# Kernel optimization log

Hardware: AMD Instinct MI355X
Metric: run time of the kernel (lower is better)

## Reference

```python
import jax, jax.numpy as jnp
import numpy as np

D = 1024
H = 16
F = 4096
EPS = 1e-6


def _layernorm(x, alpha, bias):
    # Faithful to torch: unbiased std (ddof=1), divide by (std + eps)
    mean = jnp.mean(x, axis=-1, keepdims=True)
    std = jnp.std(x, axis=-1, keepdims=True, ddof=1)
    return alpha * (x - mean) / (std + EPS) + bias


def setup_inputs() -> dict:
    key = jax.random.key(0)
    ks = jax.random.split(key, 12)
    B, S = 2, 2048
    s = 1.0 / np.sqrt(D)
    inp = {
        "x": jax.random.normal(ks[0], (B, S, D), jnp.float32),
        "mask": jnp.ones((B, 1, 1, S), jnp.int32),
        "wq": jax.random.normal(ks[1], (D, D), jnp.float32) * s,
        "bq": jnp.zeros((D,), jnp.float32),
        "wk": jax.random.normal(ks[2], (D, D), jnp.float32) * s,
        "bk": jnp.zeros((D,), jnp.float32),
        "wv": jax.random.normal(ks[3], (D, D), jnp.float32) * s,
        "bv": jnp.zeros((D,), jnp.float32),
        "wo": jax.random.normal(ks[4], (D, D), jnp.float32) * s,
        "bo": jnp.zeros((D,), jnp.float32),
        "ln1_a": jnp.ones((D,), jnp.float32),
        "ln1_b": jnp.zeros((D,), jnp.float32),
        "ln2_a": jnp.ones((D,), jnp.float32),
        "ln2_b": jnp.zeros((D,), jnp.float32),
        "w1": jax.random.normal(ks[5], (D, F), jnp.float32) * s,
        "b1": jnp.zeros((F,), jnp.float32),
        "w2": jax.random.normal(ks[6], (F, D), jnp.float32) * (1.0 / np.sqrt(F)),
        "b2": jnp.zeros((D,), jnp.float32),
    }
    return inp


def reference(x, mask, wq, bq, wk, bk, wv, bv, wo, bo,
              ln1_a, ln1_b, ln2_a, ln2_b, w1, b1, w2, b2):
    B, S, _ = x.shape
    dk = D // H
    # --- residual 1: pre-LN self-attention ---
    h = _layernorm(x, ln1_a, ln1_b)
    q = (h @ wq + bq).reshape(B, S, H, dk).transpose(0, 2, 1, 3)
    k = (h @ wk + bk).reshape(B, S, H, dk).transpose(0, 2, 1, 3)
    v = (h @ wv + bv).reshape(B, S, H, dk).transpose(0, 2, 1, 3)
    scores = jnp.einsum('bhqd,bhkd->bhqk', q, k) / jnp.sqrt(jnp.float32(dk))
    scores = jnp.where(mask == 0, jnp.float32(-1e9), scores)
    attn = jax.nn.softmax(scores, axis=-1)
    ctx = jnp.einsum('bhqk,bhkd->bhqd', attn, v)
    ctx = ctx.transpose(0, 2, 1, 3).reshape(B, S, D)
    x = x + (ctx @ wo + bo)
    # --- residual 2: pre-LN feed-forward ---
    h = _layernorm(x, ln2_a, ln2_b)
    ff = jax.nn.relu(h @ w1 + b1) @ w2 + b2
    return x + ff
```

## Files before the change

kernel.cpp:

```cpp
#include <hip/hip_runtime.h>
#include <hip/hip_bf16.h>
#include <math.h>

typedef __attribute__((ext_vector_type(8))) short bf16x8;
typedef __attribute__((ext_vector_type(4))) float f32x4;
typedef unsigned int uint32;
typedef __attribute__((ext_vector_type(2))) unsigned int uint32x2;

#define DMODEL 1024
#define SEQ    2048
#define NB     2
#define NH     16
#define HD     64
#define FDIM   4096
#define NTOK   (NB*SEQ)

__device__ __forceinline__ void async16(const void* g, void* s) {
    __builtin_amdgcn_global_load_lds((const __attribute__((address_space(1))) unsigned int*)g,
                                     (__attribute__((address_space(3))) unsigned int*)s,
                                     16, 0, 0);
}

__global__ __launch_bounds__(256) void transpose_cvt_k(const float* __restrict__ src,
                                                       __hip_bfloat16* __restrict__ dst,
                                                       int R, int C) {
    __shared__ __hip_bfloat16 tile[32][33];
    int tx = threadIdx.x, ty = threadIdx.y;
    int bx = blockIdx.x * 32, by = blockIdx.y * 32;
    for (int i = 0; i < 32; i += 8)
        tile[ty + i][tx] = __float2bfloat16(src[(size_t)(by + ty + i) * C + bx + tx]);
    __syncthreads();
    for (int i = 0; i < 32; i += 8)
        dst[(size_t)(bx + ty + i) * R + by + tx] = tile[tx][ty + i];
}

__global__ __launch_bounds__(256) void transpose_cvt4_k(const float* __restrict__ s0,
                                                        const float* __restrict__ s1,
                                                        const float* __restrict__ s2,
                                                        const float* __restrict__ s3,
                                                        __hip_bfloat16* __restrict__ d012,
                                                        __hip_bfloat16* __restrict__ d3) {
    __shared__ __hip_bfloat16 tile[32][33];
    const int z = blockIdx.z;
    const float* src = (z == 0) ? s0 : (z == 1) ? s1 : (z == 2) ? s2 : s3;
    __hip_bfloat16* dst = (z < 3) ? d012 + (size_t)z * DMODEL * DMODEL : d3;
    int tx = threadIdx.x, ty = threadIdx.y;
    int bx = blockIdx.x * 32, by = blockIdx.y * 32;
    for (int i = 0; i < 32; i += 8)
        tile[ty + i][tx] = __float2bfloat16(src[(size_t)(by + ty + i) * DMODEL + bx + tx]);
    __syncthreads();
    for (int i = 0; i < 32; i += 8)
        dst[(size_t)(bx + ty + i) * DMODEL + by + tx] = tile[tx][ty + i];
}

__global__ __launch_bounds__(256) void ln_kernel(const float* __restrict__ x,
                                                 const float* __restrict__ alpha,
                                                 const float* __restrict__ beta,
                                                 __hip_bfloat16* __restrict__ out) {
    const int row = blockIdx.x, tid = threadIdx.x;
    const size_t base = (size_t)row * DMODEL;
    float v[4];
    for (int e = 0; e < 4; ++e) v[e] = x[base + tid * 4 + e];
    float s1 = v[0] + v[1] + v[2] + v[3];
    float s2 = v[0]*v[0] + v[1]*v[1] + v[2]*v[2] + v[3]*v[3];
    for (int off = 32; off > 0; off >>= 1) {
        s1 += __shfl_down(s1, off);
        s2 += __shfl_down(s2, off);
    }
    __shared__ float red[8];
    int w = tid >> 6, lane = tid & 63;
    if (lane == 0) { red[w * 2] = s1; red[w * 2 + 1] = s2; }
    __syncthreads();
    if (tid == 0) {
        float a = 0.f, b = 0.f;
        for (int i = 0; i < 4; ++i) { a += red[2 * i]; b += red[2 * i + 1]; }
        red[0] = a; red[1] = b;
    }
    __syncthreads();
    s1 = red[0]; s2 = red[1];
    float mean = s1 * (1.0f / DMODEL);
    float var  = fmaxf((s2 - (float)DMODEL * mean * mean) * (1.0f / (DMODEL - 1)), 0.f);
    float inv  = 1.0f / (sqrtf(var) + 1e-6f);
    for (int e = 0; e < 4; ++e) {
        int c = tid * 4 + e;
        float y = alpha[c] * (v[e] - mean) * inv + beta[c];
        out[base + c] = __float2bfloat16(y);
    }
}

template <int EPI>
__global__ __launch_bounds__(256) void gemm_bt(const __hip_bfloat16* __restrict__ A,
                                               const __hip_bfloat16* __restrict__ Bt,
                                               const float* __restrict__ bias,
                                               const float* __restrict__ res,
                                               void* __restrict__ Cout,
                                               int M, int N, int K) {
    __shared__ alignas(16) __hip_bfloat16 As[2][128 * 32];
    __shared__ alignas(16) __hip_bfloat16 Bs[2][128 * 32];
    const int tid = threadIdx.x, l = tid & 63;
    const int w = tid >> 6;
    const int wm = w >> 1, wn = w & 1, quad = l >> 4, lc = l & 15;
    const int row0 = blockIdx.y * 128, col0 = blockIdx.x * 128;
    const int lr = l >> 2, cb = l & 3;
    const int srow = 32 * w + lr;
    const int scol = (cb ^ ((lr >> 1) & 3)) * 8;
    const int rsw  = (lc >> 1) & 3;

    f32x4 acc[4][4];
    for (int i = 0; i < 4; ++i)
        for (int j = 0; j < 4; ++j) acc[i][j] = (f32x4){0.f, 0.f, 0.f, 0.f};

    for (int c = 0; c < 2; ++c) {
        async16(A  + (size_t)(row0 + srow + 16 * c) * K + scol, (char*)&As[0][0] + w * 2048 + c * 1024);
        async16(Bt + (size_t)(col0 + srow + 16 * c) * K + scol, (char*)&Bs[0][0] + w * 2048 + c * 1024);
    }
    const int NKT = K / 32;
    for (int kt = 0; kt < NKT; ++kt) {
        const int cur = kt & 1;
        __syncthreads();
        if (kt + 1 < NKT) {
            const int k1 = (kt + 1) * 32;
            for (int c = 0; c < 2; ++c) {
                async16(A  + (size_t)(row0 + srow + 16 * c) * K + k1 + scol, (char*)&As[cur ^ 1][0] + w * 2048 + c * 1024);
                async16(Bt + (size_t)(col0 + srow + 16 * c) * K + k1 + scol, (char*)&Bs[cur ^ 1][0] + w * 2048 + c * 1024);
            }
        }
        bf16x8 af[4], bfr[4];
        for (int i = 0; i < 4; ++i) af[i]  = *(const bf16x8*)&As[cur][(64 * wm + 16 * i + lc) * 32 + (quad ^ rsw) * 8];
        for (int j = 0; j < 4; ++j) bfr[j] = *(const bf16x8*)&Bs[cur][(64 * wn + 16 * j + lc) * 32 + (quad ^ rsw) * 8];
        for (int i = 0; i < 4; ++i)
            for (int j = 0; j < 4; ++j)
                acc[i][j] = __builtin_amdgcn_mfma_f32_16x16x32_bf16(af[i], bfr[j], acc[i][j], 0, 0, 0);
    }

    __hip_bfloat16* Cb = (__hip_bfloat16*)Cout;
    float* Cf = (float*)Cout;
    for (int j = 0; j < 4; ++j) {
        int col = col0 + 64 * wn + 16 * j + lc;
        float bv = bias[col];
        for (int i = 0; i < 4; ++i) {
            int rbase = row0 + 64 * wm + 16 * i + quad * 4;
            for (int r = 0; r < 4; ++r) {
                size_t idx = (size_t)(rbase + r) * N + col;
                float vacc = acc[i][j][r] + bv;
                if (EPI == 0)      Cb[idx] = __float2bfloat16(vacc);
                else if (EPI == 1) Cb[idx] = __float2bfloat16(fmaxf(vacc, 0.f));
                else               Cf[idx] = vacc + res[idx];
            }
        }
    }
}

template <int EPI>
__global__ __launch_bounds__(512) void gemm_bt_sk(const __hip_bfloat16* __restrict__ A,
                                                  const __hip_bfloat16* __restrict__ Bt,
                                                  const float* __restrict__ bias,
                                                  const float* __restrict__ res,
                                                  void* __restrict__ Cout,
                                                  int M, int N, int K) {
    __shared__ alignas(16) char smem[65536];
    const int tid = threadIdx.x, l = tid & 63;
    const int w = tid >> 6;
    const int g = w >> 2;
    const int wl = w & 3;
    const int wm = wl >> 1, wn = wl & 1, quad = l >> 4, lc = l & 15;
    const int row0 = blockIdx.y * 128, col0 = blockIdx.x * 128;
    const int lr = l >> 2, cb = l & 3;
    const int srow = 32 * wl + lr;
    const int scol = (cb ^ ((lr >> 1) & 3)) * 8;
    const int rsw  = (lc >> 1) & 3;
    const int Kh = K >> 1;
    const int kbase = g * Kh;

    char* AsBase = smem + (size_t)g * 16384;
    char* BsBase = smem + 32768 + (size_t)g * 16384;

    f32x4 acc[4][4];
    for (int i = 0; i < 4; ++i)
        for (int j = 0; j < 4; ++j) acc[i][j] = (f32x4){0.f, 0.f, 0.f, 0.f};

    for (int c = 0; c < 2; ++c) {
        async16(A  + (size_t)(row0 + srow + 16 * c) * K + kbase + scol, AsBase + wl * 2048 + c * 1024);
        async16(Bt + (size_t)(col0 + srow + 16 * c) * K + kbase + scol, BsBase + wl * 2048 + c * 1024);
    }
    const int NKT = Kh / 32;
    for (int kt = 0; kt < NKT; ++kt) {
        const int cur = kt & 1;
        __syncthreads();
        if (kt + 1 < NKT) {
            const int k1 = kbase + (kt + 1) * 32;
            for (int c = 0; c < 2; ++c) {
                async16(A  + (size_t)(row0 + srow + 16 * c) * K + k1 + scol, AsBase + (cur ^ 1) * 8192 + wl * 2048 + c * 1024);
                async16(Bt + (size_t)(col0 + srow + 16 * c) * K + k1 + scol, BsBase + (cur ^ 1) * 8192 + wl * 2048 + c * 1024);
            }
        }
        const __hip_bfloat16* Asc = (const __hip_bfloat16*)(AsBase + cur * 8192);
        const __hip_bfloat16* Bsc = (const __hip_bfloat16*)(BsBase + cur * 8192);
        bf16x8 af[4], bfr[4];
        for (int i = 0; i < 4; ++i) af[i]  = *(const bf16x8*)&Asc[(64 * wm + 16 * i + lc) * 32 + (quad ^ rsw) * 8];
        for (int j = 0; j < 4; ++j) bfr[j] = *(const bf16x8*)&Bsc[(64 * wn + 16 * j + lc) * 32 + (quad ^ rsw) * 8];
        for (int i = 0; i < 4; ++i)
            for (int j = 0; j < 4; ++j)
                acc[i][j] = __builtin_amdgcn_mfma_f32_16x16x32_bf16(af[i], bfr[j], acc[i][j], 0, 0, 0);
    }

    __syncthreads();
    float* comb = (float*)smem;
    if (g == 1) {
        for (int j = 0; j < 4; ++j) {
            int col = 64 * wn + 16 * j + lc;
            int ccol = col ^ ((quad & 1) << 4);
            for (int i = 0; i < 4; ++i) {
                int rb = 64 * wm + 16 * i + quad * 4;
                for (int r = 0; r < 4; ++r)
                    comb[(rb + r) * 128 + ccol] = acc[i][j][r];
            }
        }
    }
    __syncthreads();
    if (g == 0) {
        __hip_bfloat16* Cb = (__hip_bfloat16*)Cout;
        float* Cf = (float*)Cout;
        for (int j = 0; j < 4; ++j) {
            int coll = 64 * wn + 16 * j + lc;
            int ccol = coll ^ ((quad & 1) << 4);
            int col  = col0 + coll;
            float bv = bias[col];
            for (int i = 0; i < 4; ++i) {
                int rbl = 64 * wm + 16 * i + quad * 4;
                for (int r = 0; r < 4; ++r) {
                    size_t idx = (size_t)(row0 + rbl + r) * N + col;
                    float vacc = acc[i][j][r] + comb[(rbl + r) * 128 + ccol] + bv;
                    if (EPI == 0)      Cb[idx] = __float2bfloat16(vacc);
                    else if (EPI == 1) Cb[idx] = __float2bfloat16(fmaxf(vacc, 0.f));
                    else               Cf[idx] = vacc + res[idx];
                }
            }
        }
    }
}

__global__ __launch_bounds__(256) void gemm_qkv(const __hip_bfloat16* __restrict__ A,
                                                const __hip_bfloat16* __restrict__ Bt,
                                                const float* __restrict__ bq,
                                                const float* __restrict__ bk,
                                                const float* __restrict__ bv,
                                                __hip_bfloat16* __restrict__ qout,
                                                __hip_bfloat16* __restrict__ kout,
                                                __hip_bfloat16* __restrict__ vTout) {
    const int K = DMODEL;
    __shared__ alignas(16) __hip_bfloat16 As[2][128 * 32];
    __shared__ alignas(16) __hip_bfloat16 Bs[2][128 * 32];
    const int tid = threadIdx.x, l = tid & 63;
    const int w = tid >> 6;
    const int wm = w >> 1, wn = w & 1, quad = l >> 4, lc = l & 15;
    const int row0 = blockIdx.y * 128, col0 = blockIdx.x * 128;
    const int lr = l >> 2, cb = l & 3;
    const int srow = 32 * w + lr;
    const int scol = (cb ^ ((lr >> 1) & 3)) * 8;
    const int rsw  = (lc >> 1) & 3;

    f32x4 acc[4][4];
    for (int i = 0; i < 4; ++i)
        for (int j = 0; j < 4; ++j) acc[i][j] = (f32x4){0.f, 0.f, 0.f, 0.f};

    for (int c = 0; c < 2; ++c) {
        async16(A  + (size_t)(row0 + srow + 16 * c) * K + scol, (char*)&As[0][0] + w * 2048 + c * 1024);
        async16(Bt + (size_t)(col0 + srow + 16 * c) * K + scol, (char*)&Bs[0][0] + w * 2048 + c * 1024);
    }
    const int NKT = K / 32;
    for (int kt = 0; kt < NKT; ++kt) {
        const int cur = kt & 1;
        __syncthreads();
        if (kt + 1 < NKT) {
            const int k1 = (kt + 1) * 32;
            for (int c = 0; c < 2; ++c) {
                async16(A  + (size_t)(row0 + srow + 16 * c) * K + k1 + scol, (char*)&As[cur ^ 1][0] + w * 2048 + c * 1024);
                async16(Bt + (size_t)(col0 + srow + 16 * c) * K + k1 + scol, (char*)&Bs[cur ^ 1][0] + w * 2048 + c * 1024);
            }
        }
        bf16x8 af[4], bfr[4];
        for (int i = 0; i < 4; ++i) af[i]  = *(const bf16x8*)&As[cur][(64 * wm + 16 * i + lc) * 32 + (quad ^ rsw) * 8];
        for (int j = 0; j < 4; ++j) bfr[j] = *(const bf16x8*)&Bs[cur][(64 * wn + 16 * j + lc) * 32 + (quad ^ rsw) * 8];
        for (int i = 0; i < 4; ++i)
            for (int j = 0; j < 4; ++j)
                acc[i][j] = __builtin_amdgcn_mfma_f32_16x16x32_bf16(af[i], bfr[j], acc[i][j], 0, 0, 0);
    }

    const int seg = col0 >> 10;
    const float* bias = (seg == 0) ? bq : (seg == 1) ? bk : bv;
    for (int j = 0; j < 4; ++j) {
        int col  = col0 + 64 * wn + 16 * j + lc;
        int colm = col & (DMODEL - 1);
        float bvx = bias[colm];
        for (int i = 0; i < 4; ++i) {
            int rbase = row0 + 64 * wm + 16 * i + quad * 4;
            for (int r = 0; r < 4; ++r) {
                int trow = rbase + r;
                float vacc = acc[i][j][r] + bvx;
                if (seg == 2) {
                    int bb = trow >> 11, s = trow & (SEQ - 1);
                    int hh = colm >> 6, d = colm & (HD - 1);
                    vTout[((size_t)(bb * NH + hh) * HD + d) * SEQ + s] = __float2bfloat16(vacc);
                } else {
                    __hip_bfloat16* dst = (seg == 0) ? qout : kout;
                    dst[(size_t)trow * DMODEL + colm] = __float2bfloat16(vacc);
                }
            }
        }
    }
}

__global__ __launch_bounds__(512) void attn_kernel(const __hip_bfloat16* __restrict__ q,
                                                   const __hip_bfloat16* __restrict__ k,
                                                   const __hip_bfloat16* __restrict__ vT,
                                                   const int* __restrict__ mask,
                                                   __hip_bfloat16* __restrict__ ctx) {
    const int qt = blockIdx.x, bh = blockIdx.y;
    const int b = bh >> 4;
    const int q0 = qt * 128;
    const int tid = threadIdx.x, w = tid >> 6, l = tid & 63, quad = l >> 4, lc = l & 15;
    const int g = w >> 2, wl = w & 3;

    __shared__ alignas(16) char smem[65536];
    __hip_bfloat16* KhB = (__hip_bfloat16*)(smem + (size_t)g * 32768);
    __hip_bfloat16* VhB = (__hip_bfloat16*)(smem + (size_t)g * 32768 + 16384);

    const size_t base   = (size_t)b * SEQ * DMODEL + (size_t)(bh & 15) * HD;
    const size_t vtbase = (size_t)bh * HD * SEQ;
    const int gk = g * (SEQ / 2);

    bf16x8 qf[2][2];
    for (int s = 0; s < 2; ++s) {
        const __hip_bfloat16* qrow = &q[base + (size_t)(q0 + s * 64 + wl * 16 + lc) * DMODEL];
        qf[s][0] = *(const bf16x8*)&qrow[quad * 8];
        qf[s][1] = *(const bf16x8*)&qrow[32 + quad * 8];
    }

    f32x4 o[2][4];
    for (int s = 0; s < 2; ++s)
        for (int dj = 0; dj < 4; ++dj) o[s][dj] = (f32x4){0.f, 0.f, 0.f, 0.f};
    float rsp2[2] = {0.f, 0.f};

    const int lr  = l >> 2, cb = l & 3;
    const int cbsw = ((cb ^ ((lr >> 1) & 3))) * 8;
    const int rsw  = (lc >> 1) & 3;

    for (int c = 0; c < 2; ++c) {
        const int W = wl * 2 + c;
        const int rr = (W & 3) * 16 + lr, cc8 = (W >> 2) * 32 + cbsw;
        async16(&k [base   + (size_t)(gk + rr) * DMODEL + cc8], (char*)KhB + W * 1024);
        async16(&vT[vtbase + (size_t)rr * SEQ + gk + cc8],      (char*)VhB + W * 1024);
    }

    const int NT = SEQ / 128;
    for (int kt = 0; kt < NT; ++kt) {
        const int k0 = gk + kt * 64;
        const int cur = kt & 1;

        __syncthreads();
        if (kt + 1 < NT) {
            const int k1 = k0 + 64;
            for (int c = 0; c < 2; ++c) {
                const int W = wl * 2 + c;
                const int rr = (W & 3) * 16 + lr, cc8 = (W >> 2) * 32 + cbsw;
                async16(&k [base   + (size_t)(k1 + rr) * DMODEL + cc8], (char*)KhB + (cur ^ 1) * 8192 + W * 1024);
                async16(&vT[vtbase + (size_t)rr * SEQ + k1 + cc8],      (char*)VhB + (cur ^ 1) * 8192 + W * 1024);
            }
        }
        float mb[4][4];
        for (int jn = 0; jn < 4; ++jn) {
            int4 mi = *(const int4*)&mask[b * SEQ + k0 + jn * 16 + quad * 4];
            mb[jn][0] = mi.x ? 0.f : -INFINITY;
            mb[jn][1] = mi.y ? 0.f : -INFINITY;
            mb[jn][2] = mi.z ? 0.f : -INFINITY;
            mb[jn][3] = mi.w ? 0.f : -INFINITY;
        }

        bf16x8 kf0[4], kf1[4];
        for (int jn = 0; jn < 4; ++jn) {
            kf0[jn] = *(const bf16x8*)&KhB[(cur * 2 + 0) * 2048 + (jn * 16 + lc) * 32 + (quad ^ rsw) * 8];
            kf1[jn] = *(const bf16x8*)&KhB[(cur * 2 + 1) * 2048 + (jn * 16 + lc) * 32 + (quad ^ rsw) * 8];
        }
        bf16x8 vf0[4], vf1[4];
        for (int dj = 0; dj < 4; ++dj) {
            vf0[dj] = *(const bf16x8*)&VhB[(cur * 2 + 0) * 2048 + (dj * 16 + lc) * 32 + (quad ^ rsw) * 8];
            vf1[dj] = *(const bf16x8*)&VhB[(cur * 2 + 1) * 2048 + (dj * 16 + lc) * 32 + (quad ^ rsw) * 8];
        }

        for (int s = 0; s < 2; ++s) {
            f32x4 sa[4];
            __builtin_amdgcn_s_setprio(1);
            for (int jn = 0; jn < 4; ++jn) {
                f32x4 z = (f32x4){0.f, 0.f, 0.f, 0.f};
                z = __builtin_amdgcn_mfma_f32_16x16x32_bf16(kf0[jn], qf[s][0], z, 0, 0, 0);
                z = __builtin_amdgcn_mfma_f32_16x16x32_bf16(kf1[jn], qf[s][1], z, 0, 0, 0);
                sa[jn] = z;
            }
            __builtin_amdgcn_s_setprio(0);

            uint32 wd[4][2];
            float accs = 0.f;
            for (int jn = 0; jn < 4; ++jn) {
                float p0 = __expf(fmaf(sa[jn][0], 0.125f, mb[jn][0]));
                float p1 = __expf(fmaf(sa[jn][1], 0.125f, mb[jn][1]));
                float p2 = __expf(fmaf(sa[jn][2], 0.125f, mb[jn][2]));
                float p3 = __expf(fmaf(sa[jn][3], 0.125f, mb[jn][3]));
                accs += (p0 + p1) + (p2 + p3);
                __hip_bfloat16 h0 = __float2bfloat16(p0), h1 = __float2bfloat16(p1);
                __hip_bfloat16 h2 = __float2bfloat16(p2), h3 = __float2bfloat16(p3);
                wd[jn][0] = (uint32)*(unsigned short*)&h0 | ((uint32)*(unsigned short*)&h1 << 16);
                wd[jn][1] = (uint32)*(unsigned short*)&h2 | ((uint32)*(unsigned short*)&h3 << 16);
            }
            rsp2[s] += accs;

            union { uint32 u[4]; bf16x8 v8; } pf0, pf1;
            for (int p = 0; p < 2; ++p) {
                uint32x2 a = __builtin_amdgcn_permlane32_swap(wd[0][p], wd[1][p], false, false);
                uint32x2 r = __builtin_amdgcn_permlane16_swap(a[0], a[1], false, false);
                pf0.u[p] = r[0]; pf0.u[2 + p] = r[1];
                uint32x2 a2 = __builtin_amdgcn_permlane32_swap(wd[2][p], wd[3][p], false, false);
                uint32x2 r2 = __builtin_amdgcn_permlane16_swap(a2[0], a2[1], false, false);
                pf1.u[p] = r2[0]; pf1.u[2 + p] = r2[1];
            }

            __builtin_amdgcn_s_setprio(1);
            for (int dj = 0; dj < 4; ++dj) {
                o[s][dj] = __builtin_amdgcn_mfma_f32_16x16x32_bf16(pf0.v8, vf0[dj], o[s][dj], 0, 0, 0);
                o[s][dj] = __builtin_amdgcn_mfma_f32_16x16x32_bf16(pf1.v8, vf1[dj], o[s][dj], 0, 0, 0);
            }
            __builtin_amdgcn_s_setprio(0);
        }
    }

    __syncthreads();
    float* combo = (float*)smem;
    float* crs   = (float*)(smem + 33792);
    if (g == 1) {
        for (int s = 0; s < 2; ++s) {
            crs[(wl * 64 + l) * 2 + s] = rsp2[s];
            for (int dj = 0; dj < 4; ++dj)
                for (int r = 0; r < 4; ++r)
                    combo[(s * 64 + wl * 16 + quad * 4 + r) * 66 + dj * 16 + lc] = o[s][dj][r];
        }
    }
    __syncthreads();
    if (g == 0) {
        for (int s = 0; s < 2; ++s) {
            float rs = rsp2[s] + crs[(wl * 64 + l) * 2 + s];
            rs += __shfl_xor(rs, 16);
            rs += __shfl_xor(rs, 32);
            for (int r = 0; r < 4; ++r) {
                float rq = __shfl(rs, (l & 48) | (quad * 4 + r));
                float linv = 1.0f / rq;
                int row = q0 + s * 64 + wl * 16 + quad * 4 + r;
                for (int dj = 0; dj < 4; ++dj) {
                    float ov = o[s][dj][r] + combo[(s * 64 + wl * 16 + quad * 4 + r) * 66 + dj * 16 + lc];
                    ctx[base + (size_t)row * DMODEL + dj * 16 + lc] = __float2bfloat16(ov * linv);
                }
            }
        }
    }
}

extern "C" void kernel_launch(void* const* d_in, const int* in_sizes, int n_in,
                              void* d_out, int out_size, void* d_ws, size_t ws_size,
                              hipStream_t stream) {
    const float* x    = (const float*)d_in[0];
    const int*   mask = (const int*)d_in[1];
    const float* wq = (const float*)d_in[2];
    const float* bq = (const float*)d_in[3];
    const float* wk = (const float*)d_in[4];
    const float* bk = (const float*)d_in[5];
    const float* wv = (const float*)d_in[6];
    const float* bv = (const float*)d_in[7];
    const float* wo = (const float*)d_in[8];
    const float* bo = (const float*)d_in[9];
    const float* ln1_a = (const float*)d_in[10];
    const float* ln1_b = (const float*)d_in[11];
    const float* ln2_a = (const float*)d_in[12];
    const float* ln2_b = (const float*)d_in[13];
    const float* w1 = (const float*)d_in[14];
    const float* b1 = (const float*)d_in[15];
    const float* w2 = (const float*)d_in[16];
    const float* b2 = (const float*)d_in[17];
    float* out = (float*)d_out;

    char* ws = (char*)d_ws;
    const size_t SZ_WT  = (size_t)DMODEL * DMODEL * 2;
    const size_t SZ_ACT = (size_t)NTOK * DMODEL * 2;
    const size_t SZ_WF  = (size_t)FDIM * DMODEL * 2;
    size_t off = 0;
    __hip_bfloat16* wqkvT = (__hip_bfloat16*)(ws + off); off += 3 * SZ_WT;
    __hip_bfloat16* woT   = (__hip_bfloat16*)(ws + off); off += SZ_WT;
    __hip_bfloat16* w1T   = (__hip_bfloat16*)(ws + off); off += SZ_WF;
    __hip_bfloat16* w2T   = (__hip_bfloat16*)(ws + off); off += SZ_WF;
    __hip_bfloat16* h1    = (__hip_bfloat16*)(ws + off); off += SZ_ACT;
    __hip_bfloat16* qb    = (__hip_bfloat16*)(ws + off); off += SZ_ACT;
    __hip_bfloat16* kb    = (__hip_bfloat16*)(ws + off); off += SZ_ACT;
    __hip_bfloat16* vTb   = (__hip_bfloat16*)(ws + off); off += SZ_ACT;
    __hip_bfloat16* ctx   = (__hip_bfloat16*)(ws + off); off += SZ_ACT;
    float*          x1    = (float*)(ws + off);          off += (size_t)NTOK * DMODEL * 4;
    __hip_bfloat16* h2    = (__hip_bfloat16*)(ws + off); off += SZ_ACT;
    __hip_bfloat16* ff1   = h1;

    dim3 tb(32, 8);
    transpose_cvt4_k<<<dim3(32, 32, 4), tb, 0, stream>>>(wq, wk, wv, wo, wqkvT, woT);
    transpose_cvt_k<<<dim3(128, 32), tb, 0, stream>>>(w1, w1T, DMODEL, FDIM);
    transpose_cvt_k<<<dim3(32, 128), tb, 0, stream>>>(w2, w2T, FDIM, DMODEL);

    ln_kernel<<<NTOK, 256, 0, stream>>>(x, ln1_a, ln1_b, h1);

    gemm_qkv<<<dim3(3 * DMODEL / 128, NTOK / 128), 256, 0, stream>>>(h1, wqkvT, bq, bk, bv, qb, kb, vTb);

    attn_kernel<<<dim3(SEQ / 128, NB * NH), 512, 0, stream>>>(qb, kb, vTb, mask, ctx);

    gemm_bt_sk<2><<<dim3(DMODEL / 128, NTOK / 128), 512, 0, stream>>>(ctx, woT, bo, x, x1, NTOK, DMODEL, DMODEL);

    ln_kernel<<<NTOK, 256, 0, stream>>>(x1, ln2_a, ln2_b, h2);

    gemm_bt<1><<<dim3(FDIM / 128, NTOK / 128), 256, 0, stream>>>(h2, w1T, b1, nullptr, ff1, NTOK, FDIM, DMODEL);
    gemm_bt_sk<2><<<dim3(DMODEL / 128, NTOK / 128), 512, 0, stream>>>(ff1, w2T, b2, x1, out, NTOK, DMODEL, FDIM);
}
```

Before: 393.0 us.

## Drop LDS staging and key-split in attention; load K/V fragments directly from global

The attention kernel no longer stages K and V tiles through double-buffered shared memory with async global-to-LDS loads. Each wave now reads its K and V^T MFMA fragments straight from global memory. The two-group split of the key range and the LDS combine step are also removed, so blocks shrink from 512 to 256 threads and each wave walks the full key sequence. This cuts barriers and LDS traffic, but each wave re-reads K/V through the cache with no prefetch overlap, and there is less parallelism per block.

```diff
diff --git a/kernel.cpp b/kernel.cpp
--- a/kernel.cpp
+++ b/kernel.cpp
@@ -311,7 +311,7 @@
     }
 }
 
-__global__ __launch_bounds__(512) void attn_kernel(const __hip_bfloat16* __restrict__ q,
+__global__ __launch_bounds__(256) void attn_kernel(const __hip_bfloat16* __restrict__ q,
                                                    const __hip_bfloat16* __restrict__ k,
                                                    const __hip_bfloat16* __restrict__ vT,
                                                    const int* __restrict__ mask,
@@ -320,19 +320,13 @@
     const int b = bh >> 4;
     const int q0 = qt * 128;
     const int tid = threadIdx.x, w = tid >> 6, l = tid & 63, quad = l >> 4, lc = l & 15;
-    const int g = w >> 2, wl = w & 3;
-
-    __shared__ alignas(16) char smem[65536];
-    __hip_bfloat16* KhB = (__hip_bfloat16*)(smem + (size_t)g * 32768);
-    __hip_bfloat16* VhB = (__hip_bfloat16*)(smem + (size_t)g * 32768 + 16384);
 
     const size_t base   = (size_t)b * SEQ * DMODEL + (size_t)(bh & 15) * HD;
     const size_t vtbase = (size_t)bh * HD * SEQ;
-    const int gk = g * (SEQ / 2);
 
     bf16x8 qf[2][2];
     for (int s = 0; s < 2; ++s) {
-        const __hip_bfloat16* qrow = &q[base + (size_t)(q0 + s * 64 + wl * 16 + lc) * DMODEL];
+        const __hip_bfloat16* qrow = &q[base + (size_t)(q0 + s * 64 + w * 16 + lc) * DMODEL];
         qf[s][0] = *(const bf16x8*)&qrow[quad * 8];
         qf[s][1] = *(const bf16x8*)&qrow[32 + quad * 8];
     }
@@ -342,31 +336,21 @@
         for (int dj = 0; dj < 4; ++dj) o[s][dj] = (f32x4){0.f, 0.f, 0.f, 0.f};
     float rsp2[2] = {0.f, 0.f};
 
-    const int lr  = l >> 2, cb = l & 3;
-    const int cbsw = ((cb ^ ((lr >> 1) & 3))) * 8;
-    const int rsw  = (lc >> 1) & 3;
-
-    for (int c = 0; c < 2; ++c) {
-        const int W = wl * 2 + c;
-        const int rr = (W & 3) * 16 + lr, cc8 = (W >> 2) * 32 + cbsw;
-        async16(&k [base   + (size_t)(gk + rr) * DMODEL + cc8], (char*)KhB + W * 1024);
-        async16(&vT[vtbase + (size_t)rr * SEQ + gk + cc8],      (char*)VhB + W * 1024);
-    }
-
-    const int NT = SEQ / 128;
+    const int NT = SEQ / 64;
     for (int kt = 0; kt < NT; ++kt) {
-        const int k0 = gk + kt * 64;
-        const int cur = kt & 1;
-
-        __syncthreads();
-        if (kt + 1 < NT) {
-            const int k1 = k0 + 64;
-            for (int c = 0; c < 2; ++c) {
-                const int W = wl * 2 + c;
-                const int rr = (W & 3) * 16 + lr, cc8 = (W >> 2) * 32 + cbsw;
-                async16(&k [base   + (size_t)(k1 + rr) * DMODEL + cc8], (char*)KhB + (cur ^ 1) * 8192 + W * 1024);
-                async16(&vT[vtbase + (size_t)rr * SEQ + k1 + cc8],      (char*)VhB + (cur ^ 1) * 8192 + W * 1024);
-            }
+        const int k0 = kt * 64;
+
+        bf16x8 kf0[4], kf1[4];
+        for (int jn = 0; jn < 4; ++jn) {
+            const __hip_bfloat16* kr = &k[base + (size_t)(k0 + jn * 16 + lc) * DMODEL + quad * 8];
+            kf0[jn] = *(const bf16x8*)kr;
+            kf1[jn] = *(const bf16x8*)(kr + 32);
+        }
+        bf16x8 vf0[4], vf1[4];
+        for (int dj = 0; dj < 4; ++dj) {
+            const __hip_bfloat16* vr = &vT[vtbase + (size_t)(dj * 16 + lc) * SEQ + k0 + quad * 8];
+            vf0[dj] = *(const bf16x8*)vr;
+            vf1[dj] = *(const bf16x8*)(vr + 32);
         }
         float mb[4][4];
         for (int jn = 0; jn < 4; ++jn) {
@@ -375,17 +359,6 @@
             mb[jn][1] = mi.y ? 0.f : -INFINITY;
             mb[jn][2] = mi.z ? 0.f : -INFINITY;
             mb[jn][3] = mi.w ? 0.f : -INFINITY;
-        }
-
-        bf16x8 kf0[4], kf1[4];
-        for (int jn = 0; jn < 4; ++jn) {
-            kf0[jn] = *(const bf16x8*)&KhB[(cur * 2 + 0) * 2048 + (jn * 16 + lc) * 32 + (quad ^ rsw) * 8];
-            kf1[jn] = *(const bf16x8*)&KhB[(cur * 2 + 1) * 2048 + (jn * 16 + lc) * 32 + (quad ^ rsw) * 8];
-        }
-        bf16x8 vf0[4], vf1[4];
-        for (int dj = 0; dj < 4; ++dj) {
-            vf0[dj] = *(const bf16x8*)&VhB[(cur * 2 + 0) * 2048 + (dj * 16 + lc) * 32 + (quad ^ rsw) * 8];
-            vf1[dj] = *(const bf16x8*)&VhB[(cur * 2 + 1) * 2048 + (dj * 16 + lc) * 32 + (quad ^ rsw) * 8];
         }
 
         for (int s = 0; s < 2; ++s) {
@@ -433,32 +406,16 @@
         }
     }
 
-    __syncthreads();
-    float* combo = (float*)smem;
-    float* crs   = (float*)(smem + 33792);
-    if (g == 1) {
-        for (int s = 0; s < 2; ++s) {
-            crs[(wl * 64 + l) * 2 + s] = rsp2[s];
+    for (int s = 0; s < 2; ++s) {
+        float rs = rsp2[s];
+        rs += __shfl_xor(rs, 16);
+        rs += __shfl_xor(rs, 32);
+        for (int r = 0; r < 4; ++r) {
+            float rq = __shfl(rs, (l & 48) | (quad * 4 + r));
+            float linv = 1.0f / rq;
+            int row = q0 + s * 64 + w * 16 + quad * 4 + r;
             for (int dj = 0; dj < 4; ++dj)
-                for (int r = 0; r < 4; ++r)
-                    combo[(s * 64 + wl * 16 + quad * 4 + r) * 66 + dj * 16 + lc] = o[s][dj][r];
-        }
-    }
-    __syncthreads();
-    if (g == 0) {
-        for (int s = 0; s < 2; ++s) {
-            float rs = rsp2[s] + crs[(wl * 64 + l) * 2 + s];
-            rs += __shfl_xor(rs, 16);
-            rs += __shfl_xor(rs, 32);
-            for (int r = 0; r < 4; ++r) {
-                float rq = __shfl(rs, (l & 48) | (quad * 4 + r));
-                float linv = 1.0f / rq;
-                int row = q0 + s * 64 + wl * 16 + quad * 4 + r;
-                for (int dj = 0; dj < 4; ++dj) {
-                    float ov = o[s][dj][r] + combo[(s * 64 + wl * 16 + quad * 4 + r) * 66 + dj * 16 + lc];
-                    ctx[base + (size_t)row * DMODEL + dj * 16 + lc] = __float2bfloat16(ov * linv);
-                }
-            }
+                ctx[base + (size_t)row * DMODEL + dj * 16 + lc] = __float2bfloat16(o[s][dj][r] * linv);
         }
     }
 }
@@ -513,7 +470,7 @@
 
     gemm_qkv<<<dim3(3 * DMODEL / 128, NTOK / 128), 256, 0, stream>>>(h1, wqkvT, bq, bk, bv, qb, kb, vTb);
 
-    attn_kernel<<<dim3(SEQ / 128, NB * NH), 512, 0, stream>>>(qb, kb, vTb, mask, ctx);
+    attn_kernel<<<dim3(SEQ / 128, NB * NH), 256, 0, stream>>>(qb, kb, vTb, mask, ctx);
 
     gemm_bt_sk<2><<<dim3(DMODEL / 128, NTOK / 128), 512, 0, stream>>>(ctx, woT, bo, x, x1, NTOK, DMODEL, DMODEL);
 
```

New measurement: 452.5 us. +15.1%, slower.
